# Kernel tuning notes

Measured on AMD Instinct MI355X. Metric: run time of the kernel, lower is better.

## Reference

```python
import jax, jax.numpy as jnp
import numpy as np

N_NEWS, N_ENT, N_TOP = 100000, 50000, 2000
D = 128
N_EDGES = 1600000
HID, OUT = 512, 128


def setup_inputs() -> dict:
    key = jax.random.key(0)
    ks = jax.random.split(key, 12)
    return {
        "news_feats": jax.random.normal(ks[0], (N_NEWS, D), jnp.float32),
        "entity_feats": jax.random.normal(ks[1], (N_ENT, D), jnp.float32),
        "topic_feats": jax.random.normal(ks[2], (N_TOP, D), jnp.float32),
        "ent_row": jax.random.randint(ks[3], (N_EDGES,), 0, N_NEWS, jnp.int32),
        "ent_col": jax.random.randint(ks[4], (N_EDGES,), 0, N_ENT, jnp.int32),
        "top_row": jax.random.randint(ks[5], (N_EDGES,), 0, N_NEWS, jnp.int32),
        "top_col": jax.random.randint(ks[6], (N_EDGES,), 0, N_TOP, jnp.int32),
        "W1": jax.random.normal(ks[7], (3 * D, HID), jnp.float32) * 0.05,
        "b1": jnp.zeros((HID,), jnp.float32),
        "W2": jax.random.normal(ks[8], (HID, OUT), jnp.float32) * 0.05,
        "b2": jnp.zeros((OUT,), jnp.float32),
    }


def _agg(feats, row, col, num_news):
    # SpMM with binary adjacency: sum neighbor feats per news node
    gathered = feats[col]                                   # [E, D]
    summed = jax.ops.segment_sum(gathered, row, num_segments=num_news)
    deg = jax.ops.segment_sum(jnp.ones_like(row, dtype=feats.dtype), row,
                              num_segments=num_news)
    return summed / (deg[:, None] + 1e-8)


def reference(news_feats, entity_feats, topic_feats, ent_row, ent_col,
              top_row, top_col, W1, b1, W2, b2):
    n = news_feats.shape[0]
    ent_agg = _agg(entity_feats, ent_row, ent_col, n)
    top_agg = _agg(topic_feats, top_row, top_col, n)
    out = jnp.concatenate([news_feats, ent_agg, top_agg], axis=1)  # [N, 3D]
    h = jnp.tanh(out @ W1 + b1)
    return h @ W2 + b2
```

## Files before the change

### kernel.cpp

```cpp
#include <hip/hip_runtime.h>
#include <hip/hip_bf16.h>

#define NN 100000
#define NE 50000
#define NT 2000
#define DD 128
#define NEDGE 1600000
#define HID 512
#define OUTD 128
#define K1 (3*DD)
#define NBKT 391

typedef __bf16 bf16x8 __attribute__((ext_vector_type(8)));
typedef __bf16 bf16x4 __attribute__((ext_vector_type(4)));
typedef float  f32x4  __attribute__((ext_vector_type(4)));

__device__ __forceinline__ __bf16 f2b(float f) {
    __hip_bfloat16 h = __float2bfloat16(f);
    union { __hip_bfloat16 h; __bf16 b; } u; u.h = h; return u.b;
}

__device__ __forceinline__ void gll16(const void* g, void* l) {
    __builtin_amdgcn_global_load_lds((const __attribute__((address_space(1))) void*)g,
                                     (__attribute__((address_space(3))) void*)l, 16, 0, 0);
}

__device__ __forceinline__ float ftanh(float x) {
    x = fminf(fmaxf(x, -15.f), 15.f);
    float t = __expf(2.f * x);
    return (t - 1.f) / (t + 1.f);
}

__global__ void conv_feats(const float* __restrict__ entf, const float* __restrict__ topf,
                           __bf16* __restrict__ entb, __bf16* __restrict__ topb) {
    long i = ((long)blockIdx.x * 256 + threadIdx.x) * 4;
    const long NEL = (long)NE * DD;
    if (i < NEL) {
        float4 v = *(const float4*)(entf + i);
        *(bf16x4*)(entb + i) = bf16x4{f2b(v.x), f2b(v.y), f2b(v.z), f2b(v.w)};
    } else {
        long j = i - NEL;
        float4 v = *(const float4*)(topf + j);
        *(bf16x4*)(topb + j) = bf16x4{f2b(v.x), f2b(v.y), f2b(v.z), f2b(v.w)};
    }
}

__global__ __launch_bounds__(256) void hist_buckets(const int* __restrict__ er,
                                                    const int* __restrict__ tr,
                                                    int* __restrict__ bc_e,
                                                    int* __restrict__ bc_t) {
    __shared__ int lhe[NBKT], lht[NBKT];
    const int tid = threadIdx.x;
    for (int i = tid; i < NBKT; i += 256) { lhe[i] = 0; lht[i] = 0; }
    __syncthreads();
    const int base = blockIdx.x * 8192;
    #pragma unroll 4
    for (int k = 0; k < 32; k++) {
        int e = base + k * 256 + tid;
        if (e < NEDGE) {
            atomicAdd(&lhe[er[e] >> 8], 1);
            atomicAdd(&lht[tr[e] >> 8], 1);
        }
    }
    __syncthreads();
    for (int i = tid; i < NBKT; i += 256) {
        if (lhe[i]) atomicAdd(&bc_e[i], lhe[i]);
        if (lht[i]) atomicAdd(&bc_t[i], lht[i]);
    }
}

__global__ void scan_buckets(int* __restrict__ bc_e, int* __restrict__ bc_t,
                             int* __restrict__ cur_e, int* __restrict__ cur_t,
                             int* __restrict__ offs_e, int* __restrict__ offs_t) {
    int* bc  = blockIdx.y ? bc_t : bc_e;
    int* cur = blockIdx.y ? cur_t : cur_e;
    int* offs = blockIdx.y ? offs_t : offs_e;
    __shared__ int s[512];
    int i = threadIdx.x;
    s[i] = (i < NBKT) ? bc[i] : 0;
    __syncthreads();
    #pragma unroll
    for (int off = 1; off < 512; off <<= 1) {
        int v = (i >= off) ? s[i - off] : 0;
        __syncthreads();
        s[i] += v;
        __syncthreads();
    }
    if (i < NBKT) {
        bc[i] = s[i];
        cur[i] = i ? s[i - 1] : 0;
    }
    if (i == 0) offs[0] = 0;
}

__global__ __launch_bounds__(256) void scatter_bucket(const int* __restrict__ er,
                                                      const int* __restrict__ ec,
                                                      const int* __restrict__ tr,
                                                      const int* __restrict__ tc,
                                                      int* __restrict__ cur_e,
                                                      int* __restrict__ cur_t,
                                                      int* __restrict__ be,
                                                      int* __restrict__ bt) {
    __shared__ int lhe[NBKT], lht[NBKT];
    __shared__ int lbe[NBKT], lbt[NBKT];
    const int tid = threadIdx.x;
    for (int i = tid; i < NBKT; i += 256) { lhe[i] = 0; lht[i] = 0; }
    __syncthreads();
    const int base = blockIdx.x * 4096;
    #pragma unroll 4
    for (int k = 0; k < 16; k++) {
        int e = base + k * 256 + tid;
        if (e < NEDGE) {
            atomicAdd(&lhe[er[e] >> 8], 1);
            atomicAdd(&lht[tr[e] >> 8], 1);
        }
    }
    __syncthreads();
    for (int i = tid; i < NBKT; i += 256) {
        int c = lhe[i];
        lbe[i] = c ? atomicAdd(&cur_e[i], c) : 0;
        lhe[i] = 0;
        c = lht[i];
        lbt[i] = c ? atomicAdd(&cur_t[i], c) : 0;
        lht[i] = 0;
    }
    __syncthreads();
    #pragma unroll 4
    for (int k = 0; k < 16; k++) {
        int e = base + k * 256 + tid;
        if (e < NEDGE) {
            int r = er[e];
            int b = r >> 8;
            int p = lbe[b] + atomicAdd(&lhe[b], 1);
            be[p] = ((r & 255) << 16) | ec[e];
            r = tr[e];
            b = r >> 8;
            p = lbt[b] + atomicAdd(&lht[b], 1);
            bt[p] = ((r & 255) << 16) | tc[e];
        }
    }
}

__global__ __launch_bounds__(256) void bucket_csr(const int* __restrict__ be,
                                                  const int* __restrict__ bt,
                                                  const int* __restrict__ bc_e,
                                                  const int* __restrict__ bc_t,
                                                  int* __restrict__ offs_e,
                                                  int* __restrict__ offs_t,
                                                  int* __restrict__ se,
                                                  int* __restrict__ st) {
    const int* buf = blockIdx.y ? bt : be;
    const int* bc  = blockIdx.y ? bc_t : bc_e;
    int* offs      = blockIdx.y ? offs_t : offs_e;
    int* sout      = blockIdx.y ? st : se;
    const int b = blockIdx.x;
    const int tid = threadIdx.x;
    const int start = b ? bc[b - 1] : 0;
    const int cnt = bc[b] - start;

    __shared__ int scn[256];
    __shared__ int lcur[256];
    scn[tid] = 0;
    __syncthreads();
    for (int i = tid; i < cnt; i += 256)
        atomicAdd(&scn[buf[start + i] >> 16], 1);
    __syncthreads();
    #pragma unroll
    for (int off = 1; off < 256; off <<= 1) {
        int v = (tid >= off) ? scn[tid - off] : 0;
        __syncthreads();
        scn[tid] += v;
        __syncthreads();
    }
    const int node = b * 256 + tid;
    if (node < NN) offs[node + 1] = start + scn[tid];
    lcur[tid] = start + (tid ? scn[tid - 1] : 0);
    __syncthreads();
    for (int i = tid; i < cnt; i += 256) {
        int v = buf[start + i];
        int p = atomicAdd(&lcur[v >> 16], 1);
        sout[p] = v & 0xFFFF;
    }
}

__global__ __launch_bounds__(256) void aggregate2(const float* __restrict__ news,
                                                  const __bf16* __restrict__ entb,
                                                  const __bf16* __restrict__ topb,
                                                  const int* __restrict__ offs_e,
                                                  const int* __restrict__ offs_t,
                                                  const int* __restrict__ se,
                                                  const int* __restrict__ st,
                                                  __bf16* __restrict__ X) {
    const int wave = threadIdx.x >> 6, lane = threadIdx.x & 63;
    const int node = blockIdx.x * 4 + wave;
    if (node >= NN) return;
    const int h = lane >> 4;
    const int d = (lane & 15) * 8;

    float ea[8] = {0,0,0,0,0,0,0,0};
    float pa[8] = {0,0,0,0,0,0,0,0};

    const int s0 = offs_e[node], s1 = offs_e[node + 1];
    int i = s0 + h;
    for (; i + 12 < s1; i += 16) {
        int c0 = se[i], c1 = se[i + 4], c2 = se[i + 8], c3 = se[i + 12];
        bf16x8 v0 = *(const bf16x8*)(entb + (long)c0 * DD + d);
        bf16x8 v1 = *(const bf16x8*)(entb + (long)c1 * DD + d);
        bf16x8 v2 = *(const bf16x8*)(entb + (long)c2 * DD + d);
        bf16x8 v3 = *(const bf16x8*)(entb + (long)c3 * DD + d);
        #pragma unroll
        for (int j = 0; j < 8; j++)
            ea[j] += ((float)v0[j] + (float)v1[j]) + ((float)v2[j] + (float)v3[j]);
    }
    for (; i < s1; i += 4) {
        bf16x8 v = *(const bf16x8*)(entb + (long)se[i] * DD + d);
        #pragma unroll
        for (int j = 0; j < 8; j++) ea[j] += (float)v[j];
    }

    const int t0 = offs_t[node], t1 = offs_t[node + 1];
    i = t0 + h;
    for (; i + 12 < t1; i += 16) {
        int c0 = st[i], c1 = st[i + 4], c2 = st[i + 8], c3 = st[i + 12];
        bf16x8 v0 = *(const bf16x8*)(topb + (long)c0 * DD + d);
        bf16x8 v1 = *(const bf16x8*)(topb + (long)c1 * DD + d);
        bf16x8 v2 = *(const bf16x8*)(topb + (long)c2 * DD + d);
        bf16x8 v3 = *(const bf16x8*)(topb + (long)c3 * DD + d);
        #pragma unroll
        for (int j = 0; j < 8; j++)
            pa[j] += ((float)v0[j] + (float)v1[j]) + ((float)v2[j] + (float)v3[j]);
    }
    for (; i < t1; i += 4) {
        bf16x8 v = *(const bf16x8*)(topb + (long)st[i] * DD + d);
        #pragma unroll
        for (int j = 0; j < 8; j++) pa[j] += (float)v[j];
    }

    #pragma unroll
    for (int j = 0; j < 8; j++) {
        ea[j] += __shfl_xor(ea[j], 16, 64);
        ea[j] += __shfl_xor(ea[j], 32, 64);
        pa[j] += __shfl_xor(pa[j], 16, 64);
        pa[j] += __shfl_xor(pa[j], 32, 64);
    }

    const float ie = 1.0f / ((float)(s1 - s0) + 1e-8f);
    const float it = 1.0f / ((float)(t1 - t0) + 1e-8f);
    __bf16* xr = X + (long)node * K1;
    if (h == 0) {
        float4 n0 = *(const float4*)(news + (long)node * DD + d);
        float4 n1 = *(const float4*)(news + (long)node * DD + d + 4);
        *(bf16x8*)(xr + d) = bf16x8{f2b(n0.x), f2b(n0.y), f2b(n0.z), f2b(n0.w),
                                    f2b(n1.x), f2b(n1.y), f2b(n1.z), f2b(n1.w)};
    } else if (h == 1) {
        *(bf16x8*)(xr + DD + d) = bf16x8{f2b(ea[0]*ie), f2b(ea[1]*ie), f2b(ea[2]*ie), f2b(ea[3]*ie),
                                         f2b(ea[4]*ie), f2b(ea[5]*ie), f2b(ea[6]*ie), f2b(ea[7]*ie)};
    } else if (h == 2) {
        *(bf16x8*)(xr + 2*DD + d) = bf16x8{f2b(pa[0]*it), f2b(pa[1]*it), f2b(pa[2]*it), f2b(pa[3]*it),
                                           f2b(pa[4]*it), f2b(pa[5]*it), f2b(pa[6]*it), f2b(pa[7]*it)};
    }
}

__global__ void conv_w(const float* __restrict__ W1, const float* __restrict__ W2,
                       __bf16* __restrict__ W1T, __bf16* __restrict__ W2T) {
    int i = blockIdx.x * 256 + threadIdx.x;
    if (i < K1 * HID) {
        int k = i / HID, n = i % HID;
        W1T[n * K1 + k] = f2b(W1[i]);
    } else {
        int j = i - K1 * HID;
        if (j < HID * OUTD) {
            int k = j / OUTD, n = j % OUTD;
            W2T[n * HID + k] = f2b(W2[j]);
        }
    }
}


__device__ __forceinline__ void stage_tile(const __bf16* __restrict__ src, int ldK,
                                           int k0, int row0, int rowmax,
                                           __bf16* lds, int w, int lane) {
    #pragma unroll
    for (int half = 0; half < 2; half++) {
        int ss = w * 64 + half * 256 + lane;
        int r = ss >> 2;
        int sw = (r & 3) ^ ((r >> 2) & 3);
        int c = (ss & 3) ^ sw;
        int gr = row0 + r; if (gr >= rowmax) gr = rowmax - 1;
        gll16(src + (long)gr * ldK + k0 + c * 8,
              lds + (w * 64 + half * 256) * 8);
    }
}

__device__ __forceinline__ bf16x8 frag(const __bf16* lds, int r, int q) {
    int sw = (r & 3) ^ ((r >> 2) & 3);
    return *(const bf16x8*)(lds + (r * 4 + (q ^ sw)) * 8);
}

__device__ __forceinline__ void hs_write(__bf16* Hs, int r, int c, __bf16 v) {
    int ch = c >> 3;
    int pch = ((((ch >> 2) ^ ((r >> 2) & 3)) << 2) | ((ch & 3) ^ (r & 3)));
    Hs[(r * 16 + pch) * 8 + (c & 7)] = v;
}
__device__ __forceinline__ bf16x8 hs_frag(const __bf16* Hs, int r, int kk, int q) {
    int pch = (((kk ^ ((r >> 2) & 3)) << 2) | (q ^ (r & 3)));
    return *(const bf16x8*)(Hs + (r * 16 + pch) * 8);
}

__global__ __launch_bounds__(256, 2) void mlp_fused(const __bf16* __restrict__ X,
                                                    const __bf16* __restrict__ W1T,
                                                    const float* __restrict__ b1,
                                                    const __bf16* __restrict__ W2T,
                                                    const float* __restrict__ b2,
                                                    float* __restrict__ out) {
    __shared__ __bf16 Xs[128 * 32];
    __shared__ __bf16 Ws[128 * 32];
    __shared__ __bf16 Hs[128 * 128];
    const int bm = blockIdx.x * 128;
    const int t = threadIdx.x;
    const int lane = t & 63;
    const int w = t >> 6;
    const int quad = lane >> 4;
    const int l16 = lane & 15;
    const int wm = w >> 1, wn = w & 1;

    f32x4 oacc[4][4];
    #pragma unroll
    for (int i = 0; i < 4; i++)
        #pragma unroll
        for (int j = 0; j < 4; j++)
            #pragma unroll
            for (int r = 0; r < 4; r++) oacc[i][j][r] = 0.0f;

    for (int nc = 0; nc < 4; nc++) {
        f32x4 hacc[4][4];
        #pragma unroll
        for (int i = 0; i < 4; i++)
            #pragma unroll
            for (int j = 0; j < 4; j++)
                #pragma unroll
                for (int r = 0; r < 4; r++) hacc[i][j][r] = 0.0f;

        for (int kt = 0; kt < K1 / 32; kt++) {
            __syncthreads();
            stage_tile(X,   K1, kt * 32, bm,       NN,  Xs, w, lane);
            stage_tile(W1T, K1, kt * 32, nc * 128, HID, Ws, w, lane);
            __syncthreads();
            bf16x8 af[4], bfr[4];
            #pragma unroll
            for (int i = 0; i < 4; i++) {
                af[i]  = frag(Xs, wm * 64 + i * 16 + l16, quad);
                bfr[i] = frag(Ws, wn * 64 + i * 16 + l16, quad);
            }
            #pragma unroll
            for (int i = 0; i < 4; i++)
                #pragma unroll
                for (int j = 0; j < 4; j++)
                    hacc[i][j] = __builtin_amdgcn_mfma_f32_16x16x32_bf16(af[i], bfr[j], hacc[i][j], 0, 0, 0);
        }

        #pragma unroll
        for (int j = 0; j < 4; j++) {
            const int col = wn * 64 + j * 16 + l16;
            const float bb = b1[nc * 128 + col];
            #pragma unroll
            for (int i = 0; i < 4; i++) {
                const int rbase = wm * 64 + i * 16 + quad * 4;
                #pragma unroll
                for (int r = 0; r < 4; r++)
                    hs_write(Hs, rbase + r, col, f2b(ftanh(hacc[i][j][r] + bb)));
            }
        }

        for (int kk = 0; kk < 4; kk++) {
            __syncthreads();
            stage_tile(W2T, HID, nc * 128 + kk * 32, 0, OUTD, Ws, w, lane);
            __syncthreads();
            bf16x8 af[4], bfr[4];
            #pragma unroll
            for (int i = 0; i < 4; i++) {
                af[i]  = hs_frag(Hs, wm * 64 + i * 16 + l16, kk, quad);
                bfr[i] = frag(Ws, wn * 64 + i * 16 + l16, quad);
            }
            #pragma unroll
            for (int i = 0; i < 4; i++)
                #pragma unroll
                for (int j = 0; j < 4; j++)
                    oacc[i][j] = __builtin_amdgcn_mfma_f32_16x16x32_bf16(af[i], bfr[j], oacc[i][j], 0, 0, 0);
        }
    }

    #pragma unroll
    for (int j = 0; j < 4; j++) {
        const int gc = wn * 64 + j * 16 + l16;
        const float bb = b2[gc];
        #pragma unroll
        for (int i = 0; i < 4; i++) {
            const int rbase = bm + wm * 64 + i * 16 + quad * 4;
            #pragma unroll
            for (int r = 0; r < 4; r++) {
                const int gr = rbase + r;
                if (gr < NN) out[(long)gr * OUTD + gc] = oacc[i][j][r] + bb;
            }
        }
    }
}

extern "C" void kernel_launch(void* const* d_in, const int* in_sizes, int n_in,
                              void* d_out, int out_size, void* d_ws, size_t ws_size,
                              hipStream_t stream) {
    const float* news  = (const float*)d_in[0];
    const float* ent_f = (const float*)d_in[1];
    const float* top_f = (const float*)d_in[2];
    const int* ent_row = (const int*)d_in[3];
    const int* ent_col = (const int*)d_in[4];
    const int* top_row = (const int*)d_in[5];
    const int* top_col = (const int*)d_in[6];
    const float* W1 = (const float*)d_in[7];
    const float* b1 = (const float*)d_in[8];
    const float* W2 = (const float*)d_in[9];
    const float* b2 = (const float*)d_in[10];

    char* ws = (char*)d_ws;
    int* offs_e = (int*)(ws + 0);
    int* offs_t = (int*)(ws + 400016);
    int* bc_e   = (int*)(ws + 800032);
    int* bc_t   = (int*)(ws + 801596);
    int* cur_e  = (int*)(ws + 803160);
    int* cur_t  = (int*)(ws + 804724);
    int* be     = (int*)(ws + 806320);
    int* bt     = (int*)(ws + 7206320);
    int* se     = (int*)(ws + 13606320);
    int* st     = (int*)(ws + 20006320);
    __bf16* entb = (__bf16*)(ws + 26406336);
    __bf16* topb = (__bf16*)(ws + 39206336);
    __bf16* X   = (__bf16*)(ws + 102400000);
    __bf16* W1T = (__bf16*)(ws + 179200000);
    __bf16* W2T = (__bf16*)(ws + 179593216);

    hipMemsetAsync(ws + 800032, 0, 6256, stream);
    conv_w<<<1024, 256, 0, stream>>>(W1, W2, W1T, W2T);
    conv_feats<<<6500, 256, 0, stream>>>(ent_f, top_f, entb, topb);
    hist_buckets<<<196, 256, 0, stream>>>(ent_row, top_row, bc_e, bc_t);
    scan_buckets<<<dim3(1, 2), 512, 0, stream>>>(bc_e, bc_t, cur_e, cur_t, offs_e, offs_t);
    scatter_bucket<<<392, 256, 0, stream>>>(ent_row, ent_col, top_row, top_col,
                                            cur_e, cur_t, be, bt);
    bucket_csr<<<dim3(NBKT, 2), 256, 0, stream>>>(be, bt, bc_e, bc_t,
                                                  offs_e, offs_t, se, st);
    aggregate2<<<NN / 4, 256, 0, stream>>>(news, entb, topb, offs_e, offs_t, se, st, X);
    mlp_fused<<<782, 256, 0, stream>>>(X, W1T, b1, W2T, b2, (float*)d_out);
}
```

Baseline: 530.6 us.

## Load MLP operand fragments directly from global into registers with double buffering

The fused MLP kernel no longer stages X, W1T and W2T tiles through shared memory with global_load_lds and per-k-step barriers. Each lane now loads its MFMA fragments straight from global memory into registers, with a two-deep register double buffer over the first GEMM's K loop. Shared memory is kept only for the hidden activation tile. This removes most __syncthreads and LDS round trips. In exchange, operands are read redundantly across waves (each X row by two waves, each weight row by every block), which raises global and L2 traffic and register pressure.

```diff
diff --git a/kernel.cpp b/kernel.cpp
--- a/kernel.cpp
+++ b/kernel.cpp
@@ -18,11 +18,6 @@
 __device__ __forceinline__ __bf16 f2b(float f) {
     __hip_bfloat16 h = __float2bfloat16(f);
     union { __hip_bfloat16 h; __bf16 b; } u; u.h = h; return u.b;
-}
-
-__device__ __forceinline__ void gll16(const void* g, void* l) {
-    __builtin_amdgcn_global_load_lds((const __attribute__((address_space(1))) void*)g,
-                                     (__attribute__((address_space(3))) void*)l, 16, 0, 0);
 }
 
 __device__ __forceinline__ float ftanh(float x) {
@@ -277,26 +272,6 @@
 }
 
 
-__device__ __forceinline__ void stage_tile(const __bf16* __restrict__ src, int ldK,
-                                           int k0, int row0, int rowmax,
-                                           __bf16* lds, int w, int lane) {
-    #pragma unroll
-    for (int half = 0; half < 2; half++) {
-        int ss = w * 64 + half * 256 + lane;
-        int r = ss >> 2;
-        int sw = (r & 3) ^ ((r >> 2) & 3);
-        int c = (ss & 3) ^ sw;
-        int gr = row0 + r; if (gr >= rowmax) gr = rowmax - 1;
-        gll16(src + (long)gr * ldK + k0 + c * 8,
-              lds + (w * 64 + half * 256) * 8);
-    }
-}
-
-__device__ __forceinline__ bf16x8 frag(const __bf16* lds, int r, int q) {
-    int sw = (r & 3) ^ ((r >> 2) & 3);
-    return *(const bf16x8*)(lds + (r * 4 + (q ^ sw)) * 8);
-}
-
 __device__ __forceinline__ void hs_write(__bf16* Hs, int r, int c, __bf16 v) {
     int ch = c >> 3;
     int pch = ((((ch >> 2) ^ ((r >> 2) & 3)) << 2) | ((ch & 3) ^ (r & 3)));
@@ -313,8 +288,6 @@
                                                     const __bf16* __restrict__ W2T,
                                                     const float* __restrict__ b2,
                                                     float* __restrict__ out) {
-    __shared__ __bf16 Xs[128 * 32];
-    __shared__ __bf16 Ws[128 * 32];
     __shared__ __bf16 Hs[128 * 128];
     const int bm = blockIdx.x * 128;
     const int t = threadIdx.x;
@@ -324,6 +297,18 @@
     const int l16 = lane & 15;
     const int wm = w >> 1, wn = w & 1;
 
+    const __bf16* Xp[4];
+    #pragma unroll
+    for (int i = 0; i < 4; i++) {
+        int r = bm + wm * 64 + i * 16 + l16;
+        if (r >= NN) r = NN - 1;
+        Xp[i] = X + (long)r * K1 + quad * 8;
+    }
+    const __bf16* W2p[4];
+    #pragma unroll
+    for (int j = 0; j < 4; j++)
+        W2p[j] = W2T + (long)(wn * 64 + j * 16 + l16) * HID + quad * 8;
+
     f32x4 oacc[4][4];
     #pragma unroll
     for (int i = 0; i < 4; i++)
@@ -333,6 +318,11 @@
             for (int r = 0; r < 4; r++) oacc[i][j][r] = 0.0f;
 
     for (int nc = 0; nc < 4; nc++) {
+        const __bf16* W1p[4];
+        #pragma unroll
+        for (int j = 0; j < 4; j++)
+            W1p[j] = W1T + (long)(nc * 128 + wn * 64 + j * 16 + l16) * K1 + quad * 8;
+
         f32x4 hacc[4][4];
         #pragma unroll
         for (int i = 0; i < 4; i++)
@@ -341,24 +331,39 @@
                 #pragma unroll
                 for (int r = 0; r < 4; r++) hacc[i][j][r] = 0.0f;
 
-        for (int kt = 0; kt < K1 / 32; kt++) {
-            __syncthreads();
-            stage_tile(X,   K1, kt * 32, bm,       NN,  Xs, w, lane);
-            stage_tile(W1T, K1, kt * 32, nc * 128, HID, Ws, w, lane);
-            __syncthreads();
-            bf16x8 af[4], bfr[4];
+        bf16x8 a0[4], b0[4], a1[4], b1f[4];
+        #pragma unroll
+        for (int i = 0; i < 4; i++) {
+            a0[i] = *(const bf16x8*)(Xp[i]);
+            b0[i] = *(const bf16x8*)(W1p[i]);
+        }
+        #pragma unroll
+        for (int kt = 0; kt < 12; kt += 2) {
             #pragma unroll
             for (int i = 0; i < 4; i++) {
-                af[i]  = frag(Xs, wm * 64 + i * 16 + l16, quad);
-                bfr[i] = frag(Ws, wn * 64 + i * 16 + l16, quad);
+                a1[i]  = *(const bf16x8*)(Xp[i]  + (kt + 1) * 32);
+                b1f[i] = *(const bf16x8*)(W1p[i] + (kt + 1) * 32);
             }
             #pragma unroll
             for (int i = 0; i < 4; i++)
                 #pragma unroll
                 for (int j = 0; j < 4; j++)
-                    hacc[i][j] = __builtin_amdgcn_mfma_f32_16x16x32_bf16(af[i], bfr[j], hacc[i][j], 0, 0, 0);
-        }
-
+                    hacc[i][j] = __builtin_amdgcn_mfma_f32_16x16x32_bf16(a0[i], b0[j], hacc[i][j], 0, 0, 0);
+            if (kt + 2 < 12) {
+                #pragma unroll
+                for (int i = 0; i < 4; i++) {
+                    a0[i] = *(const bf16x8*)(Xp[i]  + (kt + 2) * 32);
+                    b0[i] = *(const bf16x8*)(W1p[i] + (kt + 2) * 32);
+                }
+            }
+            #pragma unroll
+            for (int i = 0; i < 4; i++)
+                #pragma unroll
+                for (int j = 0; j < 4; j++)
+                    hacc[i][j] = __builtin_amdgcn_mfma_f32_16x16x32_bf16(a1[i], b1f[j], hacc[i][j], 0, 0, 0);
+        }
+
+        __syncthreads();
         #pragma unroll
         for (int j = 0; j < 4; j++) {
             const int col = wn * 64 + j * 16 + l16;
@@ -371,22 +376,22 @@
                     hs_write(Hs, rbase + r, col, f2b(ftanh(hacc[i][j][r] + bb)));
             }
         }
-
+        __syncthreads();
+
+        #pragma unroll 2
         for (int kk = 0; kk < 4; kk++) {
-            __syncthreads();
-            stage_tile(W2T, HID, nc * 128 + kk * 32, 0, OUTD, Ws, w, lane);
-            __syncthreads();
-            bf16x8 af[4], bfr[4];
-            #pragma unroll
-            for (int i = 0; i < 4; i++) {
-                af[i]  = hs_frag(Hs, wm * 64 + i * 16 + l16, kk, quad);
-                bfr[i] = frag(Ws, wn * 64 + i * 16 + l16, quad);
-            }
+            bf16x8 bw[4], ah[4];
+            #pragma unroll
+            for (int j = 0; j < 4; j++)
+                bw[j] = *(const bf16x8*)(W2p[j] + nc * 128 + kk * 32);
             #pragma unroll
             for (int i = 0; i < 4; i++)
+                ah[i] = hs_frag(Hs, wm * 64 + i * 16 + l16, kk, quad);
+            #pragma unroll
+            for (int i = 0; i < 4; i++)
                 #pragma unroll
                 for (int j = 0; j < 4; j++)
-                    oacc[i][j] = __builtin_amdgcn_mfma_f32_16x16x32_bf16(af[i], bfr[j], oacc[i][j], 0, 0, 0);
+                    oacc[i][j] = __builtin_amdgcn_mfma_f32_16x16x32_bf16(ah[i], bw[j], oacc[i][j], 0, 0, 0);
         }
     }
 
```

Result: slower. 659.3 us (+24.3%).
